# Optimization experiments

Measured on AMD Instinct MI355X. Metric: run time of the kernel, lower is better.

Reference implementation:

```python
import jax, jax.numpy as jnp
import numpy as np

NUM_GROUPS = 32
RANK = 64            # per-head rank (uniform)
IN_FEATURES = 4096
OUT_FEATURES = 4096
GROUP_DIM = OUT_FEATURES // NUM_GROUPS  # 128
SUM_RANKS = NUM_GROUPS * RANK           # 2048


def setup_inputs() -> dict:
    key = jax.random.key(0)
    k1, k2, k3 = jax.random.split(key, 3)
    hidden_states = jax.random.normal(k1, (4, 4096, IN_FEATURES), dtype=jnp.float32)
    # VT: nn.Linear(in_features, sum(ranks), bias=False) -> weight [sum_ranks, in]
    VT_weight = jax.random.normal(k2, (SUM_RANKS, IN_FEATURES), dtype=jnp.float32) * (1.0 / np.sqrt(IN_FEATURES))
    # U_list: per-group nn.Linear(r, group_dim), init.normal_ -> stacked [G, group_dim, r]
    U_weight = jax.random.normal(k3, (NUM_GROUPS, GROUP_DIM, RANK), dtype=jnp.float32)
    return {"hidden_states": hidden_states, "VT_weight": VT_weight, "U_weight": U_weight}


def reference(hidden_states, VT_weight, U_weight):
    # shared down-projection: [B,S,in] @ [in,sum_ranks] -> [B,S,sum_ranks]
    z = jnp.einsum('bsi,ri->bsr', hidden_states, VT_weight)
    B, S, _ = z.shape
    # grouped up-projection (block-diagonal GEMM): slice per group -> [B,S,G,r]
    zg = z.reshape(B, S, NUM_GROUPS, RANK)
    out = jnp.einsum('bsgr,gdr->bsgd', zg, U_weight)  # [B,S,G,group_dim]
    return out.reshape(B, S, NUM_GROUPS * GROUP_DIM)  # concat along last dim
```

## Files before the change

### kernel.cpp

```cpp
#include <hip/hip_runtime.h>
#include <hip/hip_bf16.h>
#include <stdint.h>

typedef __attribute__((ext_vector_type(8)))  short bf16x8;
typedef __attribute__((ext_vector_type(4)))  float f32x4;
typedef __attribute__((ext_vector_type(4)))  float float4v;
typedef __attribute__((ext_vector_type(8)))  unsigned short u16x8;

#define MFMA16(a,b,c) __builtin_amdgcn_mfma_f32_16x16x32_bf16((a),(b),(c),0,0,0)

__device__ __forceinline__ unsigned short f2bf(float f) {
    unsigned int u = __builtin_bit_cast(unsigned int, f);
    u = (u + 0x7fffu + ((u >> 16) & 1u)) >> 16;
    return (unsigned short)u;
}

__device__ __forceinline__ void gload_lds16(const void* g, void* l) {
    __builtin_amdgcn_global_load_lds(
        (const __attribute__((address_space(1))) void*)g,
        (__attribute__((address_space(3))) void*)l, 16, 0, 0);
}

template<int N> __device__ __forceinline__ void waitvm() {}
template<> __device__ __forceinline__ void waitvm<6>() { asm volatile("s_waitcnt vmcnt(6)" ::: "memory"); }
template<> __device__ __forceinline__ void waitvm<4>() { asm volatile("s_waitcnt vmcnt(4)" ::: "memory"); }
template<> __device__ __forceinline__ void waitvm<0>() { asm volatile("s_waitcnt vmcnt(0)" ::: "memory"); }

__global__ void cvt_f32_bf16(const float* __restrict__ in, unsigned short* __restrict__ out, long n) {
    long i = ((long)blockIdx.x * blockDim.x + threadIdx.x) * 8;
    long stride = (long)gridDim.x * blockDim.x * 8;
    for (; i < n; i += stride) {
        float4v v0 = *(const float4v*)(in + i);
        float4v v1 = *(const float4v*)(in + i + 4);
        u16x8 o;
        o[0] = f2bf(v0[0]); o[1] = f2bf(v0[1]); o[2] = f2bf(v0[2]); o[3] = f2bf(v0[3]);
        o[4] = f2bf(v1[0]); o[5] = f2bf(v1[1]); o[6] = f2bf(v1[2]); o[7] = f2bf(v1[3]);
        *(u16x8*)(out + i) = o;
    }
}


#define STAGE_A(nA_, k0n, h, l) \
    gload_lds16(pA + ((l)*128 + (h)*64) * 4096L + (k0n), (nA_) + dA0 + ((l)*128 + (h)*64) * 64)
#define STAGE_B(nB_, k0n, h, l) \
    gload_lds16(pB + ((l)*128 + (h)*32) * 4096L + (k0n), (nB_) + dB0 + ((l)*128 + (h)*32) * 64)

#define LDA(dst_, sA_, QM) do { _Pragma("unroll") for (int mi = 0; mi < 4; ++mi) { \
    dst_[mi][0] = *(const bf16x8*)((sA_) + ((wr*128 + (QM)*64 + mi*16 + lan15) << 6) + g0); \
    dst_[mi][1] = *(const bf16x8*)((sA_) + ((wr*128 + (QM)*64 + mi*16 + lan15) << 6) + (g0 ^ 32)); } } while (0)
#define LDB(dst_, sB_, QN) do { _Pragma("unroll") for (int ni = 0; ni < 2; ++ni) { \
    dst_[ni][0] = *(const bf16x8*)((sB_) + ((wc*64 + (QN)*32 + ni*16 + lan15) << 6) + g0); \
    dst_[ni][1] = *(const bf16x8*)((sB_) + ((wc*64 + (QN)*32 + ni*16 + lan15) << 6) + (g0 ^ 32)); } } while (0)

#define DOMFMA(QM, QN, aset_, bset_) do { __builtin_amdgcn_s_setprio(1); \
    _Pragma("unroll") for (int mi = 0; mi < 4; ++mi) \
      _Pragma("unroll") for (int ni = 0; ni < 2; ++ni) { \
        acc[(QM)*4+mi][(QN)*2+ni] = MFMA16(aset_[mi][0], bset_[ni][0], acc[(QM)*4+mi][(QN)*2+ni]); \
        acc[(QM)*4+mi][(QN)*2+ni] = MFMA16(aset_[mi][1], bset_[ni][1], acc[(QM)*4+mi][(QN)*2+ni]); } \
    __builtin_amdgcn_s_setprio(0); } while (0)

#define BARX() do { __builtin_amdgcn_s_barrier(); \
    asm volatile("s_waitcnt lgkmcnt(0)" ::: "memory"); \
    __builtin_amdgcn_sched_barrier(0); } while (0)
#define SB() __builtin_amdgcn_sched_barrier(0)

#define ITER8(K1, K2, K3, S2, S3, T8, V3, V7) do { \
   STAGE_A(bA1, K1, 1, 0); STAGE_A(bA1, K1, 1, 1); \
         BARX(); DOMFMA(0, 0, aE, b0); LDB(b1, bB0, 1); SB(); \
   BARX(); DOMFMA(0, 1, aE, b1); LDA(aO, bA0, 1); SB(); \
   if (S2) { STAGE_A(bA0, K2, 0, 0); STAGE_A(bA0, K2, 0, 1); \
                   STAGE_B(bB0, K2, 0, 0); STAGE_B(bB0, K2, 0, 1); } \
         BARX(); DOMFMA(1, 1, aO, b1); waitvm<V3>(); SB(); \
   if (S2) { STAGE_B(bB0, K2, 1, 0); STAGE_B(bB0, K2, 1, 1); } \
         BARX(); DOMFMA(1, 0, aO, b0); LDA(aE, bA1, 0); LDB(b0, bB1, 0); SB(); \
   if (S2) { STAGE_A(bA0, K2, 1, 0); STAGE_A(bA0, K2, 1, 1); } \
         BARX(); DOMFMA(0, 0, aE, b0); LDB(b1, bB1, 1); SB(); \
   BARX(); DOMFMA(0, 1, aE, b1); LDA(aO, bA1, 1); SB(); \
   if (S3) { STAGE_A(bA1, K3, 0, 0); STAGE_A(bA1, K3, 0, 1); \
                   STAGE_B(bB1, K3, 0, 0); STAGE_B(bB1, K3, 0, 1); } \
         BARX(); DOMFMA(1, 1, aO, b1); waitvm<V7>(); SB(); \
   if (S3) { STAGE_B(bB1, K3, 1, 0); STAGE_B(bB1, K3, 1, 1); } \
         BARX(); DOMFMA(1, 0, aO, b0); \
         if (T8) { LDA(aE, bA0, 0); LDB(b0, bB0, 0); } SB(); \
} while (0)

__global__ __launch_bounds__(512, 2) void gemm1_8ph(const unsigned short* __restrict__ A,
                                                    const unsigned short* __restrict__ B,
                                                    unsigned short* __restrict__ Z) {
    __shared__ __align__(16) unsigned short lds[65536];

    const int tid   = threadIdx.x;
    const int lane  = tid & 63;
    const int wid   = tid >> 6;
    const int wr    = wid >> 2;
    const int wc    = wid & 3;
    const int lan15 = lane & 15;
    const int g0    = (((lane >> 4) ^ (lane & 7)) << 3);

    const int  bid = blockIdx.x;
    const long m0  = (long)(bid >> 3) * 256;
    const long n0  = (long)(bid & 7) * 256;

    const int q8    = tid >> 3;
    const int granA = (((tid & 7) ^ (q8 & 7)) << 3);
    const unsigned short* pA = A + (m0 + q8) * 4096L + granA;
    const int rB0   = (q8 & 31) + ((q8 >> 5) << 6);
    const unsigned short* pB = B + (n0 + rB0) * 4096L + granA;
    const int dA0   = (wid * 8) * 64;
    const int dB0   = ((wid & 3) * 8 + ((wid >> 2) << 6)) * 64;

    f32x4 acc[8][4] = {};
    bf16x8 aE[4][2], aO[4][2], b0[2][2], b1[2][2];

    unsigned short* bA0 = lds;
    unsigned short* bB0 = lds + 16384;
    unsigned short* bA1 = lds + 32768;
    unsigned short* bB1 = lds + 49152;

    STAGE_A(bA0, 0, 0, 0);  STAGE_A(bA0, 0, 0, 1);
    STAGE_B(bB0, 0, 0, 0);  STAGE_B(bB0, 0, 0, 1);
    STAGE_B(bB0, 0, 1, 0);  STAGE_B(bB0, 0, 1, 1);
    STAGE_A(bA0, 0, 1, 0);  STAGE_A(bA0, 0, 1, 1);
    STAGE_A(bA1, 64, 0, 0); STAGE_A(bA1, 64, 0, 1);
    STAGE_B(bB1, 64, 0, 0); STAGE_B(bB1, 64, 0, 1);
    STAGE_B(bB1, 64, 1, 0); STAGE_B(bB1, 64, 1, 1);
    waitvm<6>();
    __builtin_amdgcn_s_barrier();
    __builtin_amdgcn_sched_barrier(0);
    LDA(aE, bA0, 0); LDB(b0, bB0, 0);
    SB();

    for (int i = 0; i < 31; ++i) {
        ITER8((2 * i + 1) * 64, (2 * i + 2) * 64, (2 * i + 3) * 64,
              true, true, true, 4, 4);
    }
    ITER8(63 * 64, 0, 0, false, false, false, 0, -1);

    const int rq = (lane >> 4) << 2;
    #pragma unroll
    for (int mi = 0; mi < 8; ++mi) {
        #pragma unroll
        for (int ni = 0; ni < 4; ++ni) {
            const long mb  = m0 + wr * 128 + mi * 16 + rq;
            const long nb2 = n0 + wc * 64 + ni * 16 + lan15;
            #pragma unroll
            for (int j = 0; j < 4; ++j)
                Z[(mb + j) * 2048L + nb2] = f2bf(acc[mi][ni][j]);
        }
    }
}

#define U_PAD 80

__global__ __launch_bounds__(256) void gemm2(const unsigned short* __restrict__ Z,
                                             const float* __restrict__ U,
                                             float* __restrict__ out) {
    __shared__ __align__(16) unsigned short lU[128 * U_PAD];

    const int tid  = threadIdx.x;
    const int lane = tid & 63;
    const int wid  = tid >> 6;
    const int g    = blockIdx.x & 31;
    const long m0  = (long)(blockIdx.x >> 5) * 64;

    const float* ug = U + (long)g * (128 * 64);
    for (int i = tid; i < (128 * 64) / 4; i += 256) {
        const int r = i >> 4;
        const int c = (i << 2) & 63;
        float4v v = *(const float4v*)(ug + i * 4);
        unsigned short* d = &lU[r * U_PAD + c];
        d[0] = f2bf(v[0]); d[1] = f2bf(v[1]); d[2] = f2bf(v[2]); d[3] = f2bf(v[3]);
    }
    __syncthreads();

    const long mrow = m0 + wid * 16 + (lane & 15);
    const unsigned short* zrow = Z + mrow * 2048L + g * 64 + ((lane >> 4) << 3);
    const bf16x8 a0 = *(const bf16x8*)(zrow);
    const bf16x8 a1 = *(const bf16x8*)(zrow + 32);

    f32x4 acc[8] = {};
    const int blds = (lane & 15);
    const int kofs = (lane >> 4) << 3;
    #pragma unroll
    for (int ni = 0; ni < 8; ++ni) {
        const bf16x8 c0 = *(const bf16x8*)&lU[(ni * 16 + blds) * U_PAD + kofs];
        const bf16x8 c1 = *(const bf16x8*)&lU[(ni * 16 + blds) * U_PAD + 32 + kofs];
        acc[ni] = MFMA16(a0, c0, acc[ni]);
        acc[ni] = MFMA16(a1, c1, acc[ni]);
    }

    const long mb = m0 + wid * 16 + ((lane >> 4) << 2);
    const long cb = (long)g * 128 + (lane & 15);
    #pragma unroll
    for (int ni = 0; ni < 8; ++ni)
        #pragma unroll
        for (int j = 0; j < 4; ++j)
            out[(mb + j) * 4096L + cb + ni * 16] = acc[ni][j];
}

extern "C" void kernel_launch(void* const* d_in, const int* in_sizes, int n_in,
                              void* d_out, int out_size, void* d_ws, size_t ws_size,
                              hipStream_t stream) {
    const float* hs = (const float*)d_in[0];
    const float* vt = (const float*)d_in[1];
    const float* uw = (const float*)d_in[2];
    float* out = (float*)d_out;

    unsigned short* hs_bf = (unsigned short*)d_ws;
    unsigned short* vt_bf = hs_bf + 67108864L;
    unsigned short* z_bf  = vt_bf + 8388608L;

    cvt_f32_bf16<<<2048, 256, 0, stream>>>(hs, hs_bf, 67108864L);
    cvt_f32_bf16<<<512, 256, 0, stream>>>(vt, vt_bf, 8388608L);

    gemm1_8ph<<<512, 512, 0, stream>>>(hs_bf, vt_bf, z_bf);

    gemm2<<<8192, 256, 0, stream>>>(z_bf, uw, out);
}
```

Baseline: 357.2 us.

## Fuse grouped up-projection into down-projection GEMM epilogue and merge conversion kernels

```diff
diff --git a/kernel.cpp b/kernel.cpp
--- a/kernel.cpp
+++ b/kernel.cpp
@@ -26,16 +26,30 @@
 template<> __device__ __forceinline__ void waitvm<4>() { asm volatile("s_waitcnt vmcnt(4)" ::: "memory"); }
 template<> __device__ __forceinline__ void waitvm<0>() { asm volatile("s_waitcnt vmcnt(0)" ::: "memory"); }
 
-__global__ void cvt_f32_bf16(const float* __restrict__ in, unsigned short* __restrict__ out, long n) {
-    long i = ((long)blockIdx.x * blockDim.x + threadIdx.x) * 8;
-    long stride = (long)gridDim.x * blockDim.x * 8;
-    for (; i < n; i += stride) {
-        float4v v0 = *(const float4v*)(in + i);
-        float4v v1 = *(const float4v*)(in + i + 4);
-        u16x8 o;
-        o[0] = f2bf(v0[0]); o[1] = f2bf(v0[1]); o[2] = f2bf(v0[2]); o[3] = f2bf(v0[3]);
-        o[4] = f2bf(v1[0]); o[5] = f2bf(v1[1]); o[6] = f2bf(v1[2]); o[7] = f2bf(v1[3]);
-        *(u16x8*)(out + i) = o;
+__global__ void cvt_all(const float* __restrict__ hs, const float* __restrict__ vt,
+                        unsigned short* __restrict__ hs_bf, unsigned short* __restrict__ vt_bf) {
+    if (blockIdx.x < 2048) {
+        long i = ((long)blockIdx.x * blockDim.x + threadIdx.x) * 8;
+        const long stride = 2048L * 256 * 8;
+        for (; i < 67108864L; i += stride) {
+            float4v v0 = *(const float4v*)(hs + i);
+            float4v v1 = *(const float4v*)(hs + i + 4);
+            u16x8 o;
+            o[0] = f2bf(v0[0]); o[1] = f2bf(v0[1]); o[2] = f2bf(v0[2]); o[3] = f2bf(v0[3]);
+            o[4] = f2bf(v1[0]); o[5] = f2bf(v1[1]); o[6] = f2bf(v1[2]); o[7] = f2bf(v1[3]);
+            *(u16x8*)(hs_bf + i) = o;
+        }
+    } else {
+        long i = ((long)(blockIdx.x - 2048) * blockDim.x + threadIdx.x) * 8;
+        const long stride = 512L * 256 * 8;
+        for (; i < 8388608L; i += stride) {
+            float4v v0 = *(const float4v*)(vt + i);
+            float4v v1 = *(const float4v*)(vt + i + 4);
+            u16x8 o;
+            o[0] = f2bf(v0[0]); o[1] = f2bf(v0[1]); o[2] = f2bf(v0[2]); o[3] = f2bf(v0[3]);
+            o[4] = f2bf(v1[0]); o[5] = f2bf(v1[1]); o[6] = f2bf(v1[2]); o[7] = f2bf(v1[3]);
+            *(u16x8*)(vt_bf + i) = o;
+        }
     }
 }
 
@@ -84,9 +98,10 @@
          if (T8) { LDA(aE, bA0, 0); LDB(b0, bB0, 0); } SB(); \
 } while (0)
 
-__global__ __launch_bounds__(512, 2) void gemm1_8ph(const unsigned short* __restrict__ A,
-                                                    const unsigned short* __restrict__ B,
-                                                    unsigned short* __restrict__ Z) {
+__global__ __launch_bounds__(512, 2) void gemm_fused(const unsigned short* __restrict__ A,
+                                                     const unsigned short* __restrict__ B,
+                                                     const float* __restrict__ Uw,
+                                                     float* __restrict__ out) {
     __shared__ __align__(16) unsigned short lds[65536];
 
     const int tid   = threadIdx.x;
@@ -95,6 +110,7 @@
     const int wr    = wid >> 2;
     const int wc    = wid & 3;
     const int lan15 = lane & 15;
+    const int q     = lane >> 4;
     const int g0    = (((lane >> 4) ^ (lane & 7)) << 3);
 
     const int  bid = blockIdx.x;
@@ -136,66 +152,57 @@
     }
     ITER8(63 * 64, 0, 0, false, false, false, 0, -1);
 
-    const int rq = (lane >> 4) << 2;
-    #pragma unroll
-    for (int mi = 0; mi < 8; ++mi) {
+    {
+        unsigned short* zw = lds + wid * 8192;
+
         #pragma unroll
-        for (int ni = 0; ni < 4; ++ni) {
-            const long mb  = m0 + wr * 128 + mi * 16 + rq;
-            const long nb2 = n0 + wc * 64 + ni * 16 + lan15;
+        for (int mi = 0; mi < 8; ++mi)
             #pragma unroll
-            for (int j = 0; j < 4; ++j)
-                Z[(mb + j) * 2048L + nb2] = f2bf(acc[mi][ni][j]);
+            for (int ni = 0; ni < 4; ++ni)
+                #pragma unroll
+                for (int j = 0; j < 4; ++j) {
+                    const int ml = mi * 16 + q * 4 + j;
+                    const int rr = ni * 16 + lan15;
+                    zw[ml * 64 + ((((rr >> 3)) ^ (ml & 7)) << 3) + (rr & 7)] = f2bf(acc[mi][ni][j]);
+                }
+        asm volatile("s_waitcnt lgkmcnt(0)" ::: "memory");
+        __builtin_amdgcn_sched_barrier(0);
+
+        const int g_blk = (bid & 7) * 4 + wc;
+        const float* ug = Uw + (long)g_blk * 8192;
+        const long orow0 = m0 + wr * 128;
+        const long ocol0 = (long)g_blk * 128;
+        #pragma unroll
+        for (int nf = 0; nf < 8; ++nf) {
+            bf16x8 ub[2];
+            #pragma unroll
+            for (int rk = 0; rk < 2; ++rk) {
+                const float* up = ug + (nf * 16 + lan15) * 64 + rk * 32 + q * 8;
+                float4v u0 = *(const float4v*)up;
+                float4v u1 = *(const float4v*)(up + 4);
+                u16x8 t;
+                t[0] = f2bf(u0[0]); t[1] = f2bf(u0[1]); t[2] = f2bf(u0[2]); t[3] = f2bf(u0[3]);
+                t[4] = f2bf(u1[0]); t[5] = f2bf(u1[1]); t[6] = f2bf(u1[2]); t[7] = f2bf(u1[3]);
+                ub[rk] = __builtin_bit_cast(bf16x8, t);
+            }
+            #pragma unroll
+            for (int mf = 0; mf < 8; ++mf) {
+                f32x4 o = {};
+                #pragma unroll
+                for (int rk = 0; rk < 2; ++rk) {
+                    const int ml = mf * 16 + lan15;
+                    const int gr = (rk * 4 + q) ^ (ml & 7);
+                    const bf16x8 za = *(const bf16x8*)&zw[ml * 64 + gr * 8];
+                    o = MFMA16(za, ub[rk], o);
+                }
+                const long mrow = orow0 + mf * 16 + q * 4;
+                const long ocol = ocol0 + nf * 16 + lan15;
+                #pragma unroll
+                for (int j = 0; j < 4; ++j)
+                    out[(mrow + j) * 4096L + ocol] = o[j];
+            }
         }
     }
-}
-
-#define U_PAD 80
-
-__global__ __launch_bounds__(256) void gemm2(const unsigned short* __restrict__ Z,
-                                             const float* __restrict__ U,
-                                             float* __restrict__ out) {
-    __shared__ __align__(16) unsigned short lU[128 * U_PAD];
-
-    const int tid  = threadIdx.x;
-    const int lane = tid & 63;
-    const int wid  = tid >> 6;
-    const int g    = blockIdx.x & 31;
-    const long m0  = (long)(blockIdx.x >> 5) * 64;
-
-    const float* ug = U + (long)g * (128 * 64);
-    for (int i = tid; i < (128 * 64) / 4; i += 256) {
-        const int r = i >> 4;
-        const int c = (i << 2) & 63;
-        float4v v = *(const float4v*)(ug + i * 4);
-        unsigned short* d = &lU[r * U_PAD + c];
-        d[0] = f2bf(v[0]); d[1] = f2bf(v[1]); d[2] = f2bf(v[2]); d[3] = f2bf(v[3]);
-    }
-    __syncthreads();
-
-    const long mrow = m0 + wid * 16 + (lane & 15);
-    const unsigned short* zrow = Z + mrow * 2048L + g * 64 + ((lane >> 4) << 3);
-    const bf16x8 a0 = *(const bf16x8*)(zrow);
-    const bf16x8 a1 = *(const bf16x8*)(zrow + 32);
-
-    f32x4 acc[8] = {};
-    const int blds = (lane & 15);
-    const int kofs = (lane >> 4) << 3;
-    #pragma unroll
-    for (int ni = 0; ni < 8; ++ni) {
-        const bf16x8 c0 = *(const bf16x8*)&lU[(ni * 16 + blds) * U_PAD + kofs];
-        const bf16x8 c1 = *(const bf16x8*)&lU[(ni * 16 + blds) * U_PAD + 32 + kofs];
-        acc[ni] = MFMA16(a0, c0, acc[ni]);
-        acc[ni] = MFMA16(a1, c1, acc[ni]);
-    }
-
-    const long mb = m0 + wid * 16 + ((lane >> 4) << 2);
-    const long cb = (long)g * 128 + (lane & 15);
-    #pragma unroll
-    for (int ni = 0; ni < 8; ++ni)
-        #pragma unroll
-        for (int j = 0; j < 4; ++j)
-            out[(mb + j) * 4096L + cb + ni * 16] = acc[ni][j];
 }
 
 extern "C" void kernel_launch(void* const* d_in, const int* in_sizes, int n_in,
@@ -208,12 +215,8 @@
 
     unsigned short* hs_bf = (unsigned short*)d_ws;
     unsigned short* vt_bf = hs_bf + 67108864L;
-    unsigned short* z_bf  = vt_bf + 8388608L;
-
-    cvt_f32_bf16<<<2048, 256, 0, stream>>>(hs, hs_bf, 67108864L);
-    cvt_f32_bf16<<<512, 256, 0, stream>>>(vt, vt_bf, 8388608L);
-
-    gemm1_8ph<<<512, 512, 0, stream>>>(hs_bf, vt_bf, z_bf);
-
-    gemm2<<<8192, 256, 0, stream>>>(z_bf, uw, out);
-}
+
+    cvt_all<<<2560, 256, 0, stream>>>(hs, vt, hs_bf, vt_bf);
+
+    gemm_fused<<<512, 512, 0, stream>>>(hs_bf, vt_bf, uw, out);
+}
```

Measured after the change: 387.3 us. 1.08x slower.
